# Performance work log

Hardware: AMD Instinct MI355X
Metric: run time of the kernel (lower is better)

## Reference

```python
import jax, jax.numpy as jnp
import numpy as np

N, n, m, k = 100000, 32, 16, 32
MU = 100.0  # bubble kernel scale (init arg mu)


def setup_inputs() -> dict:
    key = jax.random.key(0)
    ks = jax.random.split(key, 7)
    x = jax.random.normal(ks[0], (N,), dtype=jnp.float32)
    # torch.nn.Linear(N, n): weight [n, N], bias [n]
    encoder_w = jax.random.normal(ks[1], (n, N), dtype=jnp.float32) / np.float32(np.sqrt(N))
    encoder_b = jnp.zeros((n,), dtype=jnp.float32)
    # decoder parameter [n, N]
    decoder = jax.random.normal(ks[2], (n, N), dtype=jnp.float32) / np.float32(np.sqrt(n))
    # torch.nn.Linear(n, n*m): weight [n*m, n], bias [n*m]
    bw_w = jax.random.normal(ks[3], (n * m, n), dtype=jnp.float32) / np.float32(np.sqrt(n))
    bw_b = jnp.zeros((n * m,), dtype=jnp.float32)
    neighbour_distance = jax.random.uniform(ks[4], (N, k), dtype=jnp.float32)
    neighbour_id = jax.random.randint(ks[5], (N, k), 0, N)
    clustering_labels = jax.random.randint(ks[6], (N,), 0, m)
    return {
        "x": x,
        "encoder_w": encoder_w,
        "encoder_b": encoder_b,
        "decoder": decoder,
        "bw_w": bw_w,
        "bw_b": bw_b,
        "neighbour_distance": neighbour_distance,
        "neighbour_id": neighbour_id,
        "clustering_labels": clustering_labels,
    }


def reference(x, encoder_w, encoder_b, decoder, bw_w, bw_b,
              neighbour_distance, neighbour_id, clustering_labels):
    # encode: [N] -> [n]
    encoded = x @ encoder_w.T + encoder_b
    # per-basis, per-cluster bandwidths: sigmoid(Linear)/60 -> [n, m] -> expand to [n, N]
    bandwidths = jax.nn.sigmoid(encoded @ bw_w.T + bw_b) / 60.0
    w = bandwidths.reshape(n, m)[:, clustering_labels]  # [n, N]
    # bubble window: relu(1 - d^2 / (w*mu)^2) -> [n, N, k]
    window = jax.nn.relu(1.0 - neighbour_distance[None, :, :] ** 2
                         / (w[:, :, None] * MU) ** 2)
    # normalization over axis 1 (the N axis), faithful to the source's dim=1
    window = window / jnp.sum(window, axis=1, keepdims=True)
    # gather decoder rows at neighbours, weight, reduce over k: [n, N]
    convolved_basis = jnp.sum(decoder[:, neighbour_id] * window, axis=-1)
    # [n] @ [n, N] -> [N]
    return encoded @ convolved_basis
```

## Files before the change

### kernel.cpp

```cpp
#include <hip/hip_runtime.h>
#include <hip/hip_fp16.h>

#define N_PTS 100000
#define MU_F  100.0f
#define BUCKET 8192

typedef unsigned int uint;
typedef _Float16 h2 __attribute__((ext_vector_type(2)));
typedef float f2 __attribute__((ext_vector_type(2)));

#define E_SCALE 16384.0f
#define E_SCALE_INV (1.0f / 16384.0f)

static __device__ inline h2 h2pack(float a, float b) {
    return __builtin_bit_cast(h2, __builtin_amdgcn_cvt_pkrtz(a, b));
}
static __device__ inline float fdot2f(h2 a, h2 b, float c) {
    return __builtin_amdgcn_fdot2(a, b, c, false);
}
static __device__ inline h2 h2fma(h2 a, h2 b, h2 c) {
#if __has_builtin(__builtin_elementwise_fma)
    return __builtin_elementwise_fma(a, b, c);
#else
    return a * b + c;
#endif
}
static __device__ inline h2 h2max(h2 a, h2 b) {
#if __has_builtin(__builtin_elementwise_max)
    return __builtin_elementwise_max(a, b);
#else
    h2 r;
    r.x = a.x > b.x ? a.x : b.x;
    r.y = a.y > b.y ? a.y : b.y;
    return r;
#endif
}

#define ENC_BLKS 256
#define TR_BLKS  1563
#define SC_BLKS  98

__global__ __launch_bounds__(256) void k_prep(const float* __restrict__ x,
                                              const float* __restrict__ encW,
                                              const float* __restrict__ encB,
                                              const float* __restrict__ dec,
                                              const int* __restrict__ labels,
                                              float* __restrict__ enc,
                                              __half* __restrict__ decT,
                                              int* __restrict__ gcur,
                                              int* __restrict__ perm) {
    int b = blockIdx.x;
    if (b < ENC_BLKS) {
        int row = b & 31;
        int chunk = b >> 5;
        const int CH = N_PTS / 8;
        int base = chunk * CH;
        const float4* W4 = reinterpret_cast<const float4*>(encW + (size_t)row * N_PTS + base);
        const float4* x4 = reinterpret_cast<const float4*>(x + base);
        const int nv = CH / 4;
        float acc = 0.f;
        for (int idx = threadIdx.x; idx < nv; idx += 256) {
            float4 w = W4[idx];
            float4 xv = x4[idx];
            acc += w.x * xv.x + w.y * xv.y + w.z * xv.z + w.w * xv.w;
        }
        #pragma unroll
        for (int off = 32; off > 0; off >>= 1) acc += __shfl_down(acc, off);
        __shared__ float sred[4];
        int wid = threadIdx.x >> 6;
        if ((threadIdx.x & 63) == 0) sred[wid] = acc;
        __syncthreads();
        if (threadIdx.x == 0) {
            float s = sred[0] + sred[1] + sred[2] + sred[3];
            if (chunk == 0) s += encB[row];
            atomicAdd(enc + row, s);
        }
    } else if (b < ENC_BLKS + TR_BLKS) {
        __shared__ float tile[32][65];
        int j0 = (b - ENC_BLKS) * 64;
        int col = threadIdx.x & 63;
        int r0 = threadIdx.x >> 6;
        #pragma unroll
        for (int it = 0; it < 8; ++it) {
            int row = it * 4 + r0;
            int j = j0 + col;
            float v = (j < N_PTS) ? dec[(size_t)row * N_PTS + j] : 0.f;
            tile[row][col] = v;
        }
        __syncthreads();
        #pragma unroll
        for (int it = 0; it < 4; ++it) {
            int idx = it * 256 + threadIdx.x;
            int j = idx >> 4;
            int p = idx & 15;
            int jj = j0 + j;
            if (jj < N_PTS) {
                __half2 h = __halves2half2(__float2half(tile[2 * p][j]),
                                           __float2half(tile[2 * p + 1][j]));
                *reinterpret_cast<__half2*>(decT + (size_t)jj * 32 + 2 * p) = h;
            }
        }
    } else {
        __shared__ int lh[16], lbase[16], lcur[16];
        const int CHUNK = 1024;
        int start = (b - ENC_BLKS - TR_BLKS) * CHUNK;
        int end = min(start + CHUNK, N_PTS);
        if (threadIdx.x < 16) { lh[threadIdx.x] = 0; lcur[threadIdx.x] = 0; }
        __syncthreads();
        for (int j = start + threadIdx.x; j < end; j += 256)
            atomicAdd(&lh[labels[j]], 1);
        __syncthreads();
        if (threadIdx.x < 16)
            lbase[threadIdx.x] = threadIdx.x * BUCKET +
                                 atomicAdd(&gcur[threadIdx.x], lh[threadIdx.x]);
        __syncthreads();
        for (int j = start + threadIdx.x; j < end; j += 256) {
            int c = labels[j];
            int lpos = atomicAdd(&lcur[c], 1);
            perm[lbase[c] + lpos] = j;
        }
    }
}

__device__ inline void build_invC(const float* __restrict__ encL,
                                  const float* __restrict__ bw_w,
                                  const float* __restrict__ bw_b,
                                  float* __restrict__ invCL, int c) {
    if (threadIdx.x < 32) {
        int r = threadIdx.x * 16 + c;
        float z = bw_b[r];
        const float* wr = bw_w + r * 32;
        #pragma unroll
        for (int p = 0; p < 32; ++p) z = fmaf(encL[p], wr[p], z);
        float s = 1.f / (1.f + __expf(-z));
        float wmu = s * (MU_F / 60.0f);
        invCL[threadIdx.x] = 1.f / (wmu * wmu);
    }
}

__global__ __launch_bounds__(256, 4) void k_S_sorted(const float* __restrict__ enc_g,
                                                     const float* __restrict__ bw_w,
                                                     const float* __restrict__ bw_b,
                                                     const float* __restrict__ nd,
                                                     const int* __restrict__ perm,
                                                     const int* __restrict__ gcur,
                                                     float* __restrict__ S,
                                                     float* __restrict__ S_part) {
    __shared__ float encL[32], invCL[32];
    __shared__ float Sloc[1024];
    int b = blockIdx.x;
    int c = b & 15;
    int ch = b >> 4;
    if (threadIdx.x < 32) encL[threadIdx.x] = enc_g[threadIdx.x];
    for (int t = threadIdx.x; t < 1024; t += 256) Sloc[t] = 0.f;
    __syncthreads();
    build_invC(encL, bw_w, bw_b, invCL, c);
    __syncthreads();

    f2 inv2[16];
    #pragma unroll
    for (int t = 0; t < 16; ++t) { inv2[t].x = invCL[2 * t]; inv2[t].y = invCL[2 * t + 1]; }

    int bs = c * BUCKET;
    int cnt = gcur[c];
    int lane = threadIdx.x & 63;
    int kk = lane & 31;
    int jh = lane >> 5;
    int gw = ch * 4 + (threadIdx.x >> 6);
    const int nw = 64 * 4;
    int npairs = (cnt + 1) >> 1;

    f2 acc2[16];
    #pragma unroll
    for (int t = 0; t < 16; ++t) { acc2[t].x = 0.f; acc2[t].y = 0.f; }

    if (gw < npairs) {
        auto ld = [&](int pc, float& d, bool& v) {
            bool ok = pc < npairs;
            v = ok && (2 * pc + jh) < cnt;
            int p = v ? (bs + 2 * pc + jh) : bs;
            int j = __builtin_nontemporal_load(&perm[p]);
            d = __builtin_nontemporal_load(&nd[(size_t)j * 32 + kk]);
        };
        int pp = gw;
        float dA, dB; bool vA, vB;
        ld(pp, dA, vA);
        ld(pp + nw, dB, vB);
        while (pp < npairs) {
            float dC; bool vC;
            ld(pp + 2 * nw, dC, vC);
            float d2 = vA ? dA * dA : 1e30f;
            f2 md2; md2.x = -d2; md2.y = -d2;
            f2 onev; onev.x = 1.f; onev.y = 1.f;
            #pragma unroll
            for (int t = 0; t < 16; ++t) {
                f2 w = md2 * inv2[t] + onev;
                w.x = fmaxf(w.x, 0.f);
                w.y = fmaxf(w.y, 0.f);
                acc2[t] += w;
            }
            dA = dB; vA = vB; dB = dC; vB = vC;
            pp += nw;
        }
    }
    #pragma unroll
    for (int t = 0; t < 16; ++t) {
        acc2[t].x += __shfl_xor(acc2[t].x, 32);
        acc2[t].y += __shfl_xor(acc2[t].y, 32);
    }
    if (jh == 0) {
        #pragma unroll
        for (int t = 0; t < 16; ++t) {
            atomicAdd(&Sloc[(2 * t) * 32 + kk], acc2[t].x);
            atomicAdd(&Sloc[(2 * t + 1) * 32 + kk], acc2[t].y);
        }
    }
    __syncthreads();
    if (S_part) {
        for (int t = threadIdx.x; t < 1024; t += 256)
            S_part[(size_t)b * 1024 + t] = Sloc[t];
    } else {
        for (int t = threadIdx.x; t < 1024; t += 256) {
            float v = Sloc[t];
            if (v != 0.f) atomicAdd(&S[t], v);
        }
    }
}

__global__ __launch_bounds__(1024) void k_S_reduce(const float* __restrict__ S_part,
                                                   float* __restrict__ S) {
    int g = blockIdx.x;
    int t = threadIdx.x;
    float s = 0.f;
    #pragma unroll
    for (int u = 0; u < 16; ++u)
        s += S_part[(size_t)(g * 16 + u) * 1024 + t];
    atomicAdd(&S[t], s);
}

__global__ __launch_bounds__(256, 6) void k_main(const float* __restrict__ enc_g,
                                                 const float* __restrict__ bw_w,
                                                 const float* __restrict__ bw_b,
                                                 const float* __restrict__ S_g,
                                                 const float* __restrict__ nd,
                                                 const int* __restrict__ nid,
                                                 const int* __restrict__ perm,
                                                 const int* __restrict__ gcur,
                                                 const __half* __restrict__ decT,
                                                 float* __restrict__ out) {
    __shared__ float encL[32], invCL[32];
    __shared__ float ELf[1024];
    int c = blockIdx.x & 15;
    int ch = blockIdx.x >> 4;
    if (threadIdx.x < 32) encL[threadIdx.x] = enc_g[threadIdx.x];
    __syncthreads();
    build_invC(encL, bw_w, bw_b, invCL, c);
    for (int t = threadIdx.x; t < 1024; t += 256)
        ELf[t] = encL[t >> 5] / S_g[t] * E_SCALE;
    __syncthreads();

    int lane = threadIdx.x & 63;
    int R = lane >> 2;
    int q = lane & 3;

    h2 invh[4], EhA[4], EhB[4];
    #pragma unroll
    for (int t = 0; t < 4; ++t) {
        int i0 = q * 8 + 2 * t;
        invh[t] = h2pack(fminf(invCL[i0], 6.0e4f), fminf(invCL[i0 + 1], 6.0e4f));
        EhA[t] = h2pack(ELf[i0 * 32 + R], ELf[(i0 + 1) * 32 + R]);
        EhB[t] = h2pack(ELf[i0 * 32 + R + 16], ELf[(i0 + 1) * 32 + R + 16]);
    }
    const h2 zero2 = h2pack(0.f, 0.f);
    const h2 one2 = h2pack(1.f, 1.f);

    int bs = c * BUCKET;
    int cnt = gcur[c];
    int wv = ch * 4 + (threadIdx.x >> 6);
    const int nw = 96 * 4;
    int npairs = (cnt + 1) >> 1;
    const uint4* decQ = reinterpret_cast<const uint4*>(decT);
    if (wv >= npairs) return;

    auto load_pair = [&](int pp, int& j0, int& j1, bool& v1) {
        bool ok = pp < npairs;
        int p0 = ok ? (bs + 2 * pp) : bs;
        v1 = ok && ((2 * pp + 1) < cnt);
        j0 = perm[p0];
        j1 = perm[v1 ? p0 + 1 : p0];
    };
    auto load_ids = [&](int j0, int j1, int* id, float* dd) {
        #pragma unroll
        for (int s = 0; s < 4; ++s) {
            int jj = (s >> 1) ? j1 : j0;
            size_t idx = (size_t)jj * 32 + (s & 1) * 16 + R;
            id[s] = __builtin_nontemporal_load(&nid[idx]);
            dd[s] = __builtin_nontemporal_load(&nd[idx]);
        }
    };

    int pp = wv;
    int j0a, j1a, j0b, j1b; bool v1a, v1b;
    int ida[4]; float dda[4];
    load_pair(pp, j0a, j1a, v1a);
    load_ids(j0a, j1a, ida, dda);
    load_pair(pp + nw, j0b, j1b, v1b);

    while (pp < npairs) {
        uint4 r0 = decQ[(size_t)ida[0] * 4 + q];
        uint4 r1 = decQ[(size_t)ida[1] * 4 + q];
        uint4 r2 = decQ[(size_t)ida[2] * 4 + q];
        uint4 r3 = decQ[(size_t)ida[3] * 4 + q];
        int idb[4]; float ddb[4];
        load_ids(j0b, j1b, idb, ddb);
        int j0c, j1c; bool v1c;
        load_pair(pp + 2 * nw, j0c, j1c, v1c);

        float d20 = dda[0] * dda[0];
        float d21 = dda[1] * dda[1];
        float d22 = dda[2] * dda[2];
        float d23 = dda[3] * dda[3];
        h2 md0 = h2pack(-d20, -d20);
        h2 md1 = h2pack(-d21, -d21);
        h2 md2 = h2pack(-d22, -d22);
        h2 md3 = h2pack(-d23, -d23);

        float a0 = 0.f, a1 = 0.f, a2 = 0.f, a3 = 0.f;
        #pragma unroll
        for (int t = 0; t < 4; ++t) {
            uint dw0 = (t == 0) ? r0.x : (t == 1) ? r0.y : (t == 2) ? r0.z : r0.w;
            uint dw1 = (t == 0) ? r1.x : (t == 1) ? r1.y : (t == 2) ? r1.z : r1.w;
            uint dw2 = (t == 0) ? r2.x : (t == 1) ? r2.y : (t == 2) ? r2.z : r2.w;
            uint dw3 = (t == 0) ? r3.x : (t == 1) ? r3.y : (t == 2) ? r3.z : r3.w;
            {
                h2 w = h2max(h2fma(md0, invh[t], one2), zero2);
                a0 = fdot2f(w * EhA[t], __builtin_bit_cast(h2, dw0), a0);
            }
            {
                h2 w = h2max(h2fma(md1, invh[t], one2), zero2);
                a1 = fdot2f(w * EhB[t], __builtin_bit_cast(h2, dw1), a1);
            }
            {
                h2 w = h2max(h2fma(md2, invh[t], one2), zero2);
                a2 = fdot2f(w * EhA[t], __builtin_bit_cast(h2, dw2), a2);
            }
            {
                h2 w = h2max(h2fma(md3, invh[t], one2), zero2);
                a3 = fdot2f(w * EhB[t], __builtin_bit_cast(h2, dw3), a3);
            }
        }
        float u = a0 + a1;
        float v = a2 + a3;
        #pragma unroll
        for (int off = 32; off > 0; off >>= 1) {
            u += __shfl_xor(u, off);
            v += __shfl_xor(v, off);
        }
        if (lane == 0) out[j0a] = u * E_SCALE_INV;
        if (lane == 32 && v1a) out[j1a] = v * E_SCALE_INV;

        j0a = j0b; j1a = j1b; v1a = v1b;
        j0b = j0c; j1b = j1c; v1b = v1c;
        #pragma unroll
        for (int s = 0; s < 4; ++s) { ida[s] = idb[s]; dda[s] = ddb[s]; }
        pp += nw;
    }
}

extern "C" void kernel_launch(void* const* d_in, const int* in_sizes, int n_in,
                              void* d_out, int out_size, void* d_ws, size_t ws_size,
                              hipStream_t stream) {
    const float* x     = (const float*)d_in[0];
    const float* enc_w = (const float*)d_in[1];
    const float* enc_b = (const float*)d_in[2];
    const float* dec   = (const float*)d_in[3];
    const float* bw_w  = (const float*)d_in[4];
    const float* bw_b  = (const float*)d_in[5];
    const float* nd    = (const float*)d_in[6];
    const int*   nid   = (const int*)d_in[7];
    const int*   labels= (const int*)d_in[8];
    float* out = (float*)d_out;

    char* ws = (char*)d_ws;
    float* enc    = (float*)(ws + 0);
    float* S      = (float*)(ws + 128);
    int* gcur     = (int*)(ws + 4224);
    int* perm     = (int*)(ws + 8192);
    __half* decT  = (__half*)(ws + 532480);
    bool use_part = ws_size >= 11126784ull;
    float* S_part = use_part ? (float*)(ws + 6932480) : nullptr;

    (void)hipMemsetAsync(d_ws, 0, 4288, stream);
    k_prep<<<dim3(ENC_BLKS + TR_BLKS + SC_BLKS), dim3(256), 0, stream>>>(
        x, enc_w, enc_b, dec, labels, enc, decT, gcur, perm);
    k_S_sorted<<<dim3(1024), dim3(256), 0, stream>>>(enc, bw_w, bw_b, nd, perm,
                                                     gcur, S, S_part);
    if (use_part)
        k_S_reduce<<<dim3(64), dim3(1024), 0, stream>>>(S_part, S);
    k_main<<<dim3(1536), dim3(256), 0, stream>>>(enc, bw_w, bw_b, S, nd, nid,
                                                 perm, gcur, decT, out);
}
```

Before: 176.9 us.

## Move decoder transpose into S kernel and deepen gather prefetch in main kernel

The fp16 decoder transpose moves out of the prep kernel and into extra blocks of the S-accumulation kernel, so it runs alongside the S pass instead of the encoder and bucketing work. The main kernel now prefetches decoder rows one iteration ahead and neighbour ids two iterations ahead, a deeper software pipeline meant to hide gather latency. To make room for the extra live registers, the kernel drops to 4 waves-per-SIMD occupancy and 1024 blocks with a wave stride of 256. Fewer resident waves may reduce latency hiding elsewhere, and the longer S kernel could delay the main pass.

```diff
diff --git a/kernel.cpp b/kernel.cpp
--- a/kernel.cpp
+++ b/kernel.cpp
@@ -37,16 +37,15 @@
 }
 
 #define ENC_BLKS 256
+#define SC_BLKS  98
 #define TR_BLKS  1563
-#define SC_BLKS  98
+#define S_BLKS   1024
 
 __global__ __launch_bounds__(256) void k_prep(const float* __restrict__ x,
                                               const float* __restrict__ encW,
                                               const float* __restrict__ encB,
-                                              const float* __restrict__ dec,
                                               const int* __restrict__ labels,
                                               float* __restrict__ enc,
-                                              __half* __restrict__ decT,
                                               int* __restrict__ gcur,
                                               int* __restrict__ perm) {
     int b = blockIdx.x;
@@ -75,35 +74,10 @@
             if (chunk == 0) s += encB[row];
             atomicAdd(enc + row, s);
         }
-    } else if (b < ENC_BLKS + TR_BLKS) {
-        __shared__ float tile[32][65];
-        int j0 = (b - ENC_BLKS) * 64;
-        int col = threadIdx.x & 63;
-        int r0 = threadIdx.x >> 6;
-        #pragma unroll
-        for (int it = 0; it < 8; ++it) {
-            int row = it * 4 + r0;
-            int j = j0 + col;
-            float v = (j < N_PTS) ? dec[(size_t)row * N_PTS + j] : 0.f;
-            tile[row][col] = v;
-        }
-        __syncthreads();
-        #pragma unroll
-        for (int it = 0; it < 4; ++it) {
-            int idx = it * 256 + threadIdx.x;
-            int j = idx >> 4;
-            int p = idx & 15;
-            int jj = j0 + j;
-            if (jj < N_PTS) {
-                __half2 h = __halves2half2(__float2half(tile[2 * p][j]),
-                                           __float2half(tile[2 * p + 1][j]));
-                *reinterpret_cast<__half2*>(decT + (size_t)jj * 32 + 2 * p) = h;
-            }
-        }
     } else {
         __shared__ int lh[16], lbase[16], lcur[16];
         const int CHUNK = 1024;
-        int start = (b - ENC_BLKS - TR_BLKS) * CHUNK;
+        int start = (b - ENC_BLKS) * CHUNK;
         int end = min(start + CHUNK, N_PTS);
         if (threadIdx.x < 16) { lh[threadIdx.x] = 0; lcur[threadIdx.x] = 0; }
         __syncthreads();
@@ -145,10 +119,40 @@
                                                      const int* __restrict__ perm,
                                                      const int* __restrict__ gcur,
                                                      float* __restrict__ S,
-                                                     float* __restrict__ S_part) {
+                                                     float* __restrict__ S_part,
+                                                     const float* __restrict__ dec,
+                                                     __half* __restrict__ decT) {
+    int b = blockIdx.x;
+    if (b >= S_BLKS) {
+        __shared__ float tile[32][65];
+        int j0 = (b - S_BLKS) * 64;
+        int col = threadIdx.x & 63;
+        int r0 = threadIdx.x >> 6;
+        #pragma unroll
+        for (int it = 0; it < 8; ++it) {
+            int row = it * 4 + r0;
+            int j = j0 + col;
+            float v = (j < N_PTS) ? dec[(size_t)row * N_PTS + j] : 0.f;
+            tile[row][col] = v;
+        }
+        __syncthreads();
+        #pragma unroll
+        for (int it = 0; it < 4; ++it) {
+            int idx = it * 256 + threadIdx.x;
+            int j = idx >> 4;
+            int p = idx & 15;
+            int jj = j0 + j;
+            if (jj < N_PTS) {
+                __half2 h = __halves2half2(__float2half(tile[2 * p][j]),
+                                           __float2half(tile[2 * p + 1][j]));
+                *reinterpret_cast<__half2*>(decT + (size_t)jj * 32 + 2 * p) = h;
+            }
+        }
+        return;
+    }
+
     __shared__ float encL[32], invCL[32];
     __shared__ float Sloc[1024];
-    int b = blockIdx.x;
     int c = b & 15;
     int ch = b >> 4;
     if (threadIdx.x < 32) encL[threadIdx.x] = enc_g[threadIdx.x];
@@ -238,7 +242,7 @@
     atomicAdd(&S[t], s);
 }
 
-__global__ __launch_bounds__(256, 6) void k_main(const float* __restrict__ enc_g,
+__global__ __launch_bounds__(256, 4) void k_main(const float* __restrict__ enc_g,
                                                  const float* __restrict__ bw_w,
                                                  const float* __restrict__ bw_b,
                                                  const float* __restrict__ S_g,
@@ -277,7 +281,7 @@
     int bs = c * BUCKET;
     int cnt = gcur[c];
     int wv = ch * 4 + (threadIdx.x >> 6);
-    const int nw = 96 * 4;
+    const int NW = 64 * 4;
     int npairs = (cnt + 1) >> 1;
     const uint4* decQ = reinterpret_cast<const uint4*>(decT);
     if (wv >= npairs) return;
@@ -298,23 +302,30 @@
             dd[s] = __builtin_nontemporal_load(&nd[idx]);
         }
     };
+    auto load_rows = [&](const int* id, uint4* r) {
+        #pragma unroll
+        for (int s = 0; s < 4; ++s)
+            r[s] = decQ[(size_t)id[s] * 4 + q];
+    };
 
     int pp = wv;
-    int j0a, j1a, j0b, j1b; bool v1a, v1b;
-    int ida[4]; float dda[4];
+    int j0a, j1a, j0b, j1b, j0c, j1c; bool v1a, v1b, v1c;
+    int ida[4], idn[4]; float dda[4], ddn[4];
+    uint4 ra[4], rb[4];
+
     load_pair(pp, j0a, j1a, v1a);
     load_ids(j0a, j1a, ida, dda);
-    load_pair(pp + nw, j0b, j1b, v1b);
+    load_pair(pp + NW, j0b, j1b, v1b);
+    load_rows(ida, ra);
+    load_ids(j0b, j1b, idn, ddn);
+    load_pair(pp + 2 * NW, j0c, j1c, v1c);
 
     while (pp < npairs) {
-        uint4 r0 = decQ[(size_t)ida[0] * 4 + q];
-        uint4 r1 = decQ[(size_t)ida[1] * 4 + q];
-        uint4 r2 = decQ[(size_t)ida[2] * 4 + q];
-        uint4 r3 = decQ[(size_t)ida[3] * 4 + q];
-        int idb[4]; float ddb[4];
-        load_ids(j0b, j1b, idb, ddb);
-        int j0c, j1c; bool v1c;
-        load_pair(pp + 2 * nw, j0c, j1c, v1c);
+        load_rows(idn, rb);
+        int idc[4]; float ddc[4];
+        load_ids(j0c, j1c, idc, ddc);
+        int j0d, j1d; bool v1d;
+        load_pair(pp + 3 * NW, j0d, j1d, v1d);
 
         float d20 = dda[0] * dda[0];
         float d21 = dda[1] * dda[1];
@@ -328,10 +339,10 @@
         float a0 = 0.f, a1 = 0.f, a2 = 0.f, a3 = 0.f;
         #pragma unroll
         for (int t = 0; t < 4; ++t) {
-            uint dw0 = (t == 0) ? r0.x : (t == 1) ? r0.y : (t == 2) ? r0.z : r0.w;
-            uint dw1 = (t == 0) ? r1.x : (t == 1) ? r1.y : (t == 2) ? r1.z : r1.w;
-            uint dw2 = (t == 0) ? r2.x : (t == 1) ? r2.y : (t == 2) ? r2.z : r2.w;
-            uint dw3 = (t == 0) ? r3.x : (t == 1) ? r3.y : (t == 2) ? r3.z : r3.w;
+            uint dw0 = (t == 0) ? ra[0].x : (t == 1) ? ra[0].y : (t == 2) ? ra[0].z : ra[0].w;
+            uint dw1 = (t == 0) ? ra[1].x : (t == 1) ? ra[1].y : (t == 2) ? ra[1].z : ra[1].w;
+            uint dw2 = (t == 0) ? ra[2].x : (t == 1) ? ra[2].y : (t == 2) ? ra[2].z : ra[2].w;
+            uint dw3 = (t == 0) ? ra[3].x : (t == 1) ? ra[3].y : (t == 2) ? ra[3].z : ra[3].w;
             {
                 h2 w = h2max(h2fma(md0, invh[t], one2), zero2);
                 a0 = fdot2f(w * EhA[t], __builtin_bit_cast(h2, dw0), a0);
@@ -361,9 +372,15 @@
 
         j0a = j0b; j1a = j1b; v1a = v1b;
         j0b = j0c; j1b = j1c; v1b = v1c;
-        #pragma unroll
-        for (int s = 0; s < 4; ++s) { ida[s] = idb[s]; dda[s] = ddb[s]; }
-        pp += nw;
+        j0c = j0d; j1c = j1d; v1c = v1d;
+        #pragma unroll
+        for (int s = 0; s < 4; ++s) {
+            dda[s] = ddn[s];
+            ddn[s] = ddc[s];
+            idn[s] = idc[s];
+            ra[s] = rb[s];
+        }
+        pp += NW;
     }
 }
 
@@ -391,12 +408,12 @@
     float* S_part = use_part ? (float*)(ws + 6932480) : nullptr;
 
     (void)hipMemsetAsync(d_ws, 0, 4288, stream);
-    k_prep<<<dim3(ENC_BLKS + TR_BLKS + SC_BLKS), dim3(256), 0, stream>>>(
-        x, enc_w, enc_b, dec, labels, enc, decT, gcur, perm);
-    k_S_sorted<<<dim3(1024), dim3(256), 0, stream>>>(enc, bw_w, bw_b, nd, perm,
-                                                     gcur, S, S_part);
+    k_prep<<<dim3(ENC_BLKS + SC_BLKS), dim3(256), 0, stream>>>(
+        x, enc_w, enc_b, labels, enc, gcur, perm);
+    k_S_sorted<<<dim3(S_BLKS + TR_BLKS), dim3(256), 0, stream>>>(
+        enc, bw_w, bw_b, nd, perm, gcur, S, S_part, dec, decT);
     if (use_part)
         k_S_reduce<<<dim3(64), dim3(1024), 0, stream>>>(S_part, S);
-    k_main<<<dim3(1536), dim3(256), 0, stream>>>(enc, bw_w, bw_b, S, nd, nid,
+    k_main<<<dim3(1024), dim3(256), 0, stream>>>(enc, bw_w, bw_b, S, nd, nid,
                                                  perm, gcur, decT, out);
 }
```

New measurement: 180.2 us. About the same (+1.9%).
